# Performance work log

Hardware: AMD Instinct MI355X
Metric: run time of the kernel (lower is better)

Reference implementation:

```python
import jax, jax.numpy as jnp
import numpy as np
import math

D_MODEL = 512
NHEAD = 8
NUM_LAYERS = 3
FF_HIDDEN = 512
B, LQ, LK = 4, 1024, 2048
LN_EPS = 1e-5


def _mha(q_in, k_in, v_in, Wq, Wk, Wv, Wo, nhead, mask):
    # Weights stored [d_in, d_out]; torch Linear(bias=False) is x @ W.T, we fold the
    # transpose into storage so math is identical.
    Bq, Lq, d = q_in.shape
    dh = d // nhead
    # NOTE: original uses .view(B, nhead, -1, dh) on contiguous [B, L, d] — a plain
    # row-major reshape, NOT the usual transpose head split. Replicate exactly.
    q = (q_in @ Wq).reshape(Bq, nhead, -1, dh)
    k = (k_in @ Wk).reshape(Bq, nhead, -1, dh)
    v = (v_in @ Wv).reshape(Bq, nhead, -1, dh)
    u = jnp.einsum('bhqd,bhkd->bhqk', q, k) / math.sqrt(dh)
    if mask is not None:
        m = mask[:, None]  # broadcast over heads
        u = jnp.where(m, -jnp.inf, u)
    attn = jax.nn.softmax(u, axis=-1)
    if mask is not None:
        attn = jnp.where(m, 0.0, attn)
    out = jnp.einsum('bhqk,bhkd->bhqd', attn, v).reshape(Bq, Lq, d)
    return out @ Wo


def _layernorm(x, g, b):
    mu = jnp.mean(x, axis=-1, keepdims=True)
    var = jnp.mean((x - mu) ** 2, axis=-1, keepdims=True)
    return (x - mu) * jax.lax.rsqrt(var + LN_EPS) * g + b


def setup_inputs() -> dict:
    key = jax.random.key(0)
    ks = jax.random.split(key, 16)
    d, L, f = D_MODEL, NUM_LAYERS, FF_HIDDEN
    s = 0.02
    inp = {
        'x': jax.random.normal(ks[0], (B, LK, d), jnp.float32),
        'h': jax.random.normal(ks[1], (B, LQ, d), jnp.float32),
        'mask': jax.random.randint(ks[2], (B, LQ, LK), 0, 10) == 0,
        'wq': jax.random.normal(ks[3], (L, d, d), jnp.float32) * s,
        'wk': jax.random.normal(ks[4], (L, d, d), jnp.float32) * s,
        'wv': jax.random.normal(ks[5], (L, d, d), jnp.float32) * s,
        'wo': jax.random.normal(ks[6], (L, d, d), jnp.float32) * s,
        'ffw1': jax.random.normal(ks[7], (L, d, f), jnp.float32) * s,
        'ffb1': jnp.zeros((L, f), jnp.float32),
        'ffw2': jax.random.normal(ks[8], (L, f, d), jnp.float32) * s,
        'ffb2': jnp.zeros((L, d), jnp.float32),
        'g1': jnp.ones((L, d), jnp.float32),
        'be1': jnp.zeros((L, d), jnp.float32),
        'g2': jnp.ones((L, d), jnp.float32),
        'be2': jnp.zeros((L, d), jnp.float32),
        'out_wq': jax.random.normal(ks[9], (d, d), jnp.float32) * s,
        'out_wk': jax.random.normal(ks[10], (d, d), jnp.float32) * s,
    }
    return inp


def reference(x, h, mask, wq, wk, wv, wo, ffw1, ffb1, ffw2, ffb2, g1, be1, g2, be2, out_wq, out_wk):
    L = wq.shape[0]
    for i in range(L):
        a = _mha(h, x, x, wq[i], wk[i], wv[i], wo[i], NHEAD, mask)
        h = _layernorm(h + a, g1[i], be1[i])
        ff = jax.nn.relu(h @ ffw1[i] + ffb1[i]) @ ffw2[i] + ffb2[i]
        h = _layernorm(h + ff, g2[i], be2[i])
    # output MHA with nhead=1, output_attention=True: returns u.mean(dim=1)
    d = h.shape[-1]
    q = (h @ out_wq)[:, None]  # [B,1,Lq,d]
    k = (x @ out_wk)[:, None]  # [B,1,Lk,d]
    u = jnp.einsum('bhqd,bhkd->bhqk', q, k) / math.sqrt(d)
    # mean over head dim of size 1; torch .squeeze(1) is a no-op since Lq > 1
    return u.mean(axis=1)  # [B, Lq, Lk]
```

## Files before the change

### kernel.cpp

```cpp
#include <hip/hip_runtime.h>
#include <math.h>


#define D_MODEL 512
#define LQ 1024
#define LKK 2048
#define BB 4
#define NL 3
#define KSPLIT 2
#define NROWS 32768
#define WSZC 262144L

typedef __bf16 bf16;
typedef __bf16 bf16x8 __attribute__((ext_vector_type(8)));
typedef __bf16 bf16x4 __attribute__((ext_vector_type(4)));
typedef float f32x4 __attribute__((ext_vector_type(4)));

__device__ inline f32x4 mfma16(bf16x8 a, bf16x8 b, f32x4 c) {
    return __builtin_amdgcn_mfma_f32_16x16x32_bf16(a, b, c, 0, 0, 0);
}

__device__ inline void gload16(const void* g, void* l) {
    __builtin_amdgcn_global_load_lds(
        (const __attribute__((address_space(1))) void*)g,
        (__attribute__((address_space(3))) void*)l, 16, 0, 0);
}

__device__ inline float fexp2(float x) { return __builtin_amdgcn_exp2f(x); }

__global__ __launch_bounds__(256) void cast_kernel(
    const float* __restrict__ in, bf16* __restrict__ out, long n)
{
    long i4 = ((long)blockIdx.x * 256 + threadIdx.x) * 4;
    if (i4 >= n) return;
    float4 v = *(const float4*)(in + i4);
    bf16x4 o;
    o[0] = (bf16)v.x; o[1] = (bf16)v.y; o[2] = (bf16)v.z; o[3] = (bf16)v.w;
    *(bf16x4*)(out + i4) = o;
}

__global__ __launch_bounds__(256) void cast_dual(
    const float* __restrict__ in, float* __restrict__ outf,
    bf16* __restrict__ outb, long n)
{
    long i4 = ((long)blockIdx.x * 256 + threadIdx.x) * 4;
    if (i4 >= n) return;
    float4 v = *(const float4*)(in + i4);
    *(float4*)(outf + i4) = v;
    bf16x4 o;
    o[0] = (bf16)v.x; o[1] = (bf16)v.y; o[2] = (bf16)v.z; o[3] = (bf16)v.w;
    *(bf16x4*)(outb + i4) = o;
}

__global__ __launch_bounds__(256) void tcast_all(
    const float* __restrict__ wq, const float* __restrict__ wo,
    const float* __restrict__ f1, const float* __restrict__ f2,
    const float* __restrict__ wk, const float* __restrict__ wv,
    const float* __restrict__ owq, const float* __restrict__ owk,
    bf16* __restrict__ wts, bf16* __restrict__ wtOQ)
{
    __shared__ float t[32][33];
    int z = blockIdx.z;
    const float* src; bf16* dst;
    if (z < 3)       { src = wq  + z * WSZC;        dst = wts + (long)z * WSZC; }
    else if (z < 6)  { src = wo  + (z - 3) * WSZC;  dst = wts + (long)z * WSZC; }
    else if (z < 9)  { src = f1  + (z - 6) * WSZC;  dst = wts + (long)z * WSZC; }
    else if (z < 12) { src = f2  + (z - 9) * WSZC;  dst = wts + (long)z * WSZC; }
    else if (z < 15) { src = wk  + (z - 12) * WSZC; dst = wts + (12 + 2 * (z - 12)) * WSZC; }
    else if (z < 18) { src = wv  + (z - 15) * WSZC; dst = wts + (13 + 2 * (z - 15)) * WSZC; }
    else if (z == 18){ src = owq;                   dst = wtOQ; }
    else             { src = owk;                   dst = wts + 18 * WSZC; }

    int tx = threadIdx.x & 31, ty = threadIdx.x >> 5;
    int x0 = blockIdx.x * 32, y0 = blockIdx.y * 32;
#pragma unroll
    for (int i = 0; i < 4; i++)
        t[ty + 8 * i][tx] = src[(long)(y0 + ty + 8 * i) * 512 + x0 + tx];
    __syncthreads();
#pragma unroll
    for (int i = 0; i < 4; i++)
        dst[(long)(x0 + ty + 8 * i) * 512 + y0 + tx] = (bf16)t[tx][ty + 8 * i];
}

__global__ __launch_bounds__(256) void maskbits_kernel(
    const int* __restrict__ m, unsigned* __restrict__ bits)
{
    long i = (long)blockIdx.x * 256 + threadIdx.x;
    int v = m[i] != 0;
    unsigned long long bal = __ballot(v);
    int lane = threadIdx.x & 63;
    if (lane == 0) bits[i >> 5] = (unsigned)bal;
    else if (lane == 32) bits[i >> 5] = (unsigned)(bal >> 32);
}

__global__ __launch_bounds__(256) void vtrans_kernel(
    const bf16* __restrict__ v, bf16* __restrict__ vt)
{
    __shared__ bf16 t[64][72];
    int bh = blockIdx.y;
    int p0 = blockIdx.x * 64;
    const bf16* vb = v + ((long)bh * 2048 + p0) * 64;
    bf16* vtb = vt + (long)bh * 64 * 2048;
    int tid = threadIdx.x;
#pragma unroll
    for (int it = 0; it < 2; it++) {
        int r = it * 32 + (tid >> 3);
        int c8 = (tid & 7) * 8;
        bf16x8 vv = *(const bf16x8*)(vb + (long)r * 64 + c8);
        *(bf16x8*)&t[r][c8] = vv;
    }
    __syncthreads();
#pragma unroll
    for (int it = 0; it < 2; it++) {
        int d = it * 32 + (tid >> 3);
        int p8 = (tid & 7) * 8;
        bf16x8 ov;
#pragma unroll
        for (int j = 0; j < 8; j++) ov[j] = t[p8 + j][d];
        *(bf16x8*)(vtb + (long)d * 2048 + p0 + p8) = ov;
    }
}

template<int BIAS, int RELU, int OUT_BF16>
__global__ __launch_bounds__(256) void mfma_gemm(
    const bf16* __restrict__ A, const bf16* __restrict__ Bt,
    const float* __restrict__ bias, void* __restrict__ Cv,
    int N, int K)
{
    __shared__ bf16 As[2][8192];
    __shared__ bf16 Bs[2][4096];
    int tid = threadIdx.x;
    int lane = tid & 63, w = tid >> 6;
    int wr = w >> 1, wc = w & 1;
    int g = lane >> 4, c = lane & 15;
    long row0 = (long)blockIdx.y * 128;
    int n0 = blockIdx.x * 64;

    f32x4 acc[4][2];
#pragma unroll
    for (int m = 0; m < 4; m++)
#pragma unroll
        for (int n = 0; n < 2; n++) acc[m][n] = (f32x4){0.f, 0.f, 0.f, 0.f};

    int lr8 = lane >> 3;
    int scol = ((lane & 7) ^ lr8) * 8;
    int cs = c & 7;

    auto STAGE = [&](int buf, int k0) {
#pragma unroll
        for (int i = 0; i < 4; i++) {
            const bf16* ga = A + (row0 + w * 32 + i * 8 + lr8) * (long)K + k0 + scol;
            gload16(ga, &As[buf][(w * 32 + i * 8) * 64]);
        }
#pragma unroll
        for (int j = 0; j < 2; j++) {
            const bf16* gb = Bt + (long)(n0 + w * 16 + j * 8 + lr8) * K + k0 + scol;
            gload16(gb, &Bs[buf][(w * 16 + j * 8) * 64]);
        }
    };

    STAGE(0, 0);
    __syncthreads();
    int nk = K >> 6;
    for (int it = 0; it < nk; ++it) {
        int cur = it & 1;
        if (it + 1 < nk) STAGE(cur ^ 1, (it + 1) << 6);
#pragma unroll
        for (int kk = 0; kk < 2; kk++) {
            int ch = ((kk << 2) + g);
            bf16x8 af[4], bfr[2];
#pragma unroll
            for (int m = 0; m < 4; m++)
                af[m] = *(const bf16x8*)
                    &As[cur][(wr * 64 + m * 16 + c) * 64 + ((ch ^ cs) << 3)];
#pragma unroll
            for (int n = 0; n < 2; n++)
                bfr[n] = *(const bf16x8*)
                    &Bs[cur][(wc * 32 + n * 16 + c) * 64 + ((ch ^ cs) << 3)];
#pragma unroll
            for (int m = 0; m < 4; m++)
#pragma unroll
                for (int n = 0; n < 2; n++)
                    acc[m][n] = mfma16(af[m], bfr[n], acc[m][n]);
        }
        __syncthreads();
    }

    float bv[2] = {0.f, 0.f};
    if (BIAS) {
#pragma unroll
        for (int n = 0; n < 2; n++) bv[n] = bias[n0 + wc * 32 + n * 16 + c];
    }
    float* Cf = (float*)Cv;
    bf16* Cb = (bf16*)Cv;
#pragma unroll
    for (int m = 0; m < 4; m++)
#pragma unroll
        for (int n = 0; n < 2; n++)
#pragma unroll
            for (int j = 0; j < 4; j++) {
                long row = row0 + wr * 64 + m * 16 + g * 4 + j;
                int col = n0 + wc * 32 + n * 16 + c;
                float v = acc[m][n][j];
                if (BIAS) v += bv[n];
                if (RELU) v = fmaxf(v, 0.f);
                if (OUT_BF16) Cb[row * N + col] = (bf16)v;
                else Cf[row * N + col] = v;
            }
}

template<int OUT_BF16>
__device__ inline void gemm128_body(
    const bf16* __restrict__ Ab, const bf16* __restrict__ Bb,
    void* __restrict__ Cv, int N, int K, float scale,
    long row0, int n0)
{
    __shared__ bf16 As[2][4096];
    __shared__ bf16 Bs[2][4096];
    int tid = threadIdx.x;
    int lane = tid & 63, w = tid >> 6;
    int wr = w >> 1, wc = w & 1;
    int g = lane >> 4, c = lane & 15;

    f32x4 acc[4][4];
#pragma unroll
    for (int m = 0; m < 4; m++)
#pragma unroll
        for (int n = 0; n < 4; n++) acc[m][n] = (f32x4){0.f, 0.f, 0.f, 0.f};

    int lr4 = lane >> 2, lc8 = (lane & 3) * 8;
    auto STAGE = [&](int buf, int k0) {
        const bf16* ga = Ab + (row0 + w * 16 + lr4) * (long)K + k0 + lc8;
        gload16(ga, &As[buf][(w * 16) * 32]);
        gload16(ga + (long)64 * K, &As[buf][(w * 16 + 64) * 32]);
        const bf16* gb = Bb + (long)(n0 + w * 16 + lr4) * K + k0 + lc8;
        gload16(gb, &Bs[buf][(w * 16) * 32]);
        gload16(gb + (long)64 * K, &Bs[buf][(w * 16 + 64) * 32]);
    };

    STAGE(0, 0);
    __syncthreads();
    int nk = K >> 5;
    for (int it = 0; it < nk; ++it) {
        int cur = it & 1;
        if (it + 1 < nk) STAGE(cur ^ 1, (it + 1) << 5);
        bf16x8 af[4], bfr[4];
#pragma unroll
        for (int m = 0; m < 4; m++)
            af[m] = *(const bf16x8*)&As[cur][(wr * 64 + m * 16 + c) * 32 + g * 8];
#pragma unroll
        for (int n = 0; n < 4; n++)
            bfr[n] = *(const bf16x8*)&Bs[cur][(wc * 64 + n * 16 + c) * 32 + g * 8];
#pragma unroll
        for (int m = 0; m < 4; m++)
#pragma unroll
            for (int n = 0; n < 4; n++)
                acc[m][n] = mfma16(af[m], bfr[n], acc[m][n]);
        __syncthreads();
    }

    float* Cf = (float*)Cv;
    bf16* Cb = (bf16*)Cv;
#pragma unroll
    for (int m = 0; m < 4; m++)
#pragma unroll
        for (int n = 0; n < 4; n++)
#pragma unroll
            for (int j = 0; j < 4; j++) {
                long row = row0 + wr * 64 + m * 16 + g * 4 + j;
                int col = n0 + wc * 64 + n * 16 + c;
                float v = acc[m][n][j] * scale;
                if (OUT_BF16) Cb[row * N + col] = (bf16)v;
                else Cf[row * N + col] = v;
            }
}

__global__ __launch_bounds__(256) void mfma_gemm128(
    const bf16* __restrict__ A, const bf16* __restrict__ Bt,
    float* __restrict__ Cv, int N, int K, float scale,
    long sA, long sB, long sC)
{
    long z = blockIdx.z;
    gemm128_body<0>(A + z * sA, Bt + z * sB, Cv + z * sC, N, K, scale,
                    (long)blockIdx.y * 128, blockIdx.x * 128);
}

__global__ __launch_bounds__(256) void qkv_gemm(
    const bf16* __restrict__ Ah, const bf16* __restrict__ Ax,
    const bf16* __restrict__ B0, const bf16* __restrict__ B1,
    const bf16* __restrict__ B2,
    bf16* __restrict__ C0, bf16* __restrict__ C1, bf16* __restrict__ C2,
    float scale0)
{
    int z = blockIdx.z;
    if (z == 0 && blockIdx.y >= 32) return;
    const bf16* A = z ? Ax : Ah;
    const bf16* Bt = (z == 0) ? B0 : (z == 1 ? B1 : B2);
    bf16* C = (z == 0) ? C0 : (z == 1 ? C1 : C2);
    gemm128_body<1>(A, Bt, C, 512, 512, z == 0 ? scale0 : 1.f,
                    (long)blockIdx.y * 128, blockIdx.x * 128);
}

__global__ __launch_bounds__(512, 4) void attn_mfma(
    const bf16* __restrict__ QP, const bf16* __restrict__ KP,
    const bf16* __restrict__ Vt, const unsigned* __restrict__ bits,
    bf16* __restrict__ Opart, float* __restrict__ Mpart,
    float* __restrict__ Lpart)
{
    __shared__ bf16 Kls[2][4096];
    __shared__ bf16 Vls[2][4096];
    __shared__ bf16 Pl[8][1024];

    int tid = threadIdx.x;
    int lane = tid & 63, wv = tid >> 6;
    int g = lane >> 4, c = lane & 15;

    int flat = blockIdx.x;
    int logical = (flat & 7) * 64 + (flat >> 3);
    int bh = logical >> 4;
    int rr = logical & 15;
    int sp = rr >> 3;
    int q0 = (rr & 7) * 128 + wv * 16;
    int b = bh >> 3;

    long qrow0 = (long)bh * 1024 + q0;
    long krow0 = (long)bh * 2048 + (long)sp * 1024;
    const bf16* vtb = Vt + (long)bh * 131072 + (long)sp * 1024;
    const unsigned* bitrow = bits + ((long)b * 1024 + q0 + c) * 64 + sp * 32;

    int lr = lane >> 3, lc = lane & 7;
    int scol = (lc ^ lr) * 8;
    int cs = c & 7;

    bf16x8 qa[2];
#pragma unroll
    for (int hh = 0; hh < 2; hh++)
        qa[hh] = *(const bf16x8*)(QP + (qrow0 + c) * 64 + hh * 32 + g * 8);

    f32x4 o_acc[4];
#pragma unroll
    for (int ot = 0; ot < 4; ot++) o_acc[ot] = (f32x4){0.f, 0.f, 0.f, 0.f};
    float m_r = -1e30f, l_r = 0.f;

    {
        const bf16* sk = KP + (krow0 + wv * 8 + lr) * 64 + scol;
        gload16(sk, &Kls[0][(wv * 8) * 64]);
        const bf16* sv = vtb + (long)(wv * 8 + lr) * 2048 + scol;
        gload16(sv, &Vls[0][(wv * 8) * 64]);
    }
    uint2 wp_nxt = *(const uint2*)(bitrow);
    __syncthreads();

    const int NT = LKK / KSPLIT / 64;
    for (int kt = 0; kt < NT; kt++) {
        int cur = kt & 1;
        if (kt + 1 < NT) {
            int kn = (kt + 1) * 64;
            const bf16* sk = KP + (krow0 + kn + wv * 8 + lr) * 64 + scol;
            gload16(sk, &Kls[cur ^ 1][(wv * 8) * 64]);
            const bf16* sv = vtb + (long)(wv * 8 + lr) * 2048 + kn + scol;
            gload16(sv, &Vls[cur ^ 1][(wv * 8) * 64]);
        }
        uint2 wp = wp_nxt;
        if (kt + 1 < NT) wp_nxt = *(const uint2*)(bitrow + (kt + 1) * 2);

        const char* kls = (const char*)&Kls[cur][0];
        f32x4 s[4];
        __builtin_amdgcn_s_setprio(1);
#pragma unroll
        for (int mt = 0; mt < 4; mt++) {
            bf16x8 ka0 = *(const bf16x8*)(kls + (mt * 16 + c) * 128 + ((g ^ cs) << 4));
            bf16x8 ka1 = *(const bf16x8*)(kls + (mt * 16 + c) * 128 + (((4 + g) ^ cs) << 4));
            s[mt] = mfma16(ka0, qa[0], (f32x4){0.f, 0.f, 0.f, 0.f});
            s[mt] = mfma16(ka1, qa[1], s[mt]);
        }
        __builtin_amdgcn_s_setprio(0);

#pragma unroll
        for (int mt = 0; mt < 4; mt++)
#pragma unroll
            for (int j = 0; j < 4; j++) {
                int kl = mt * 16 + 4 * g + j;
                unsigned wsel = (kl < 32) ? wp.x : wp.y;
                if ((wsel >> (kl & 31)) & 1) s[mt][j] = -1e30f;
            }

        float mxl = -1e30f;
#pragma unroll
        for (int mt = 0; mt < 4; mt++)
            mxl = fmaxf(mxl, fmaxf(fmaxf(s[mt][0], s[mt][1]),
                                   fmaxf(s[mt][2], s[mt][3])));

        float fct = 1.f;
        if (__any(mxl > m_r + 11.5415f)) {
            float mx = fmaxf(mxl, __shfl_xor(mxl, 16, 64));
            mx = fmaxf(mx, __shfl_xor(mx, 32, 64));
            float mnew = fmaxf(m_r, mx);
            fct = fexp2(m_r - mnew);
            m_r = mnew;
            float fq[4];
#pragma unroll
            for (int j = 0; j < 4; j++)
                fq[j] = __shfl(fct, (lane & 48) | (4 * g + j), 64);
#pragma unroll
            for (int ot = 0; ot < 4; ot++)
#pragma unroll
                for (int j = 0; j < 4; j++) o_acc[ot][j] *= fq[j];
        }

        float sum = 0.f;
#pragma unroll
        for (int mt = 0; mt < 4; mt++)
#pragma unroll
            for (int j = 0; j < 4; j++) {
                float p = fexp2(s[mt][j] - m_r);
                s[mt][j] = p;
                sum += p;
            }
        sum += __shfl_xor(sum, 16, 64);
        sum += __shfl_xor(sum, 32, 64);
        l_r = l_r * fct + sum;

        char* plb = (char*)&Pl[wv][0];
#pragma unroll
        for (int mt = 0; mt < 4; mt++) {
            bf16x4 pk;
#pragma unroll
            for (int j = 0; j < 4; j++) pk[j] = (bf16)s[mt][j];
            int wch = (mt * 2 + (g >> 1)) ^ cs;
            *(bf16x4*)(plb + c * 128 + (wch << 4) + (g & 1) * 8) = pk;
        }

        const char* vls = (const char*)&Vls[cur][0];
        __builtin_amdgcn_s_setprio(1);
#pragma unroll
        for (int kh = 0; kh < 2; kh++) {
            bf16x8 pa = *(const bf16x8*)(plb + c * 128 + ((((kh << 2) + g) ^ cs) << 4));
#pragma unroll
            for (int ot = 0; ot < 4; ot++) {
                bf16x8 vbf = *(const bf16x8*)
                    (vls + (ot * 16 + c) * 128 + ((((kh << 2) + g) ^ cs) << 4));
                o_acc[ot] = mfma16(pa, vbf, o_acc[ot]);
            }
        }
        __builtin_amdgcn_s_setprio(0);
        __syncthreads();
    }

    long ob = ((long)sp * NROWS + qrow0) * 64;
#pragma unroll
    for (int ot = 0; ot < 4; ot++)
#pragma unroll
        for (int j = 0; j < 4; j++)
            Opart[ob + (long)(4 * g + j) * 64 + ot * 16 + c] = (bf16)o_acc[ot][j];
    if (g == 0) {
        Mpart[(long)sp * NROWS + qrow0 + c] = m_r;
        Lpart[(long)sp * NROWS + qrow0 + c] = l_r;
    }
}

__global__ __launch_bounds__(256) void attn_combine(
    const bf16* __restrict__ Op, const float* __restrict__ Mp,
    const float* __restrict__ Lp, bf16* __restrict__ O)
{
    long idx = (long)blockIdx.x * 256 + threadIdx.x;
    long row = idx >> 6;
    float m0 = Mp[row], m1 = Mp[NROWS + row];
    float l0 = Lp[row], l1 = Lp[NROWS + row];
    float mm = fmaxf(m0, m1);
    float e0 = fexp2(m0 - mm), e1 = fexp2(m1 - mm);
    float inv = 1.f / (l0 * e0 + l1 * e1);
    float o = ((float)Op[idx] * e0 + (float)Op[(long)NROWS * 64 + idx] * e1) * inv;
    O[idx] = (bf16)o;
}

__global__ __launch_bounds__(256) void ln_kernel(
    const float* __restrict__ res, const float* __restrict__ y,
    const float* __restrict__ g, const float* __restrict__ bb,
    float* __restrict__ outf, bf16* __restrict__ outb)
{
    int wave = threadIdx.x >> 6, lane = threadIdx.x & 63;
    long row = (long)blockIdx.x * 4 + wave;
    const float* rp = res + row * D_MODEL;
    const float* yp = y + row * D_MODEL;
    float v[8];
    float s = 0.f, sq = 0.f;
#pragma unroll
    for (int j = 0; j < 8; j++) {
        int col = lane + 64 * j;
        v[j] = rp[col] + yp[col];
        s += v[j]; sq += v[j] * v[j];
    }
#pragma unroll
    for (int o = 32; o > 0; o >>= 1) {
        s += __shfl_down(s, o, 64);
        sq += __shfl_down(sq, o, 64);
    }
    s = __shfl(s, 0, 64);
    sq = __shfl(sq, 0, 64);
    float mean = s * (1.f / 512.f);
    float var = sq * (1.f / 512.f) - mean * mean;
    float rstd = rsqrtf(fmaxf(var, 0.f) + 1e-5f);
    float* opf = outf + row * D_MODEL;
    bf16* opb = outb + row * D_MODEL;
#pragma unroll
    for (int j = 0; j < 8; j++) {
        int col = lane + 64 * j;
        float o = (v[j] - mean) * rstd * g[col] + bb[col];
        opf[col] = o;
        opb[col] = (bf16)o;
    }
}

extern "C" void kernel_launch(void* const* d_in, const int* in_sizes, int n_in,
                              void* d_out, int out_size, void* d_ws, size_t ws_size,
                              hipStream_t stream)
{
    const float* x    = (const float*)d_in[0];
    const float* hin  = (const float*)d_in[1];
    const int*   mask = (const int*)d_in[2];
    const float* wq   = (const float*)d_in[3];
    const float* wk   = (const float*)d_in[4];
    const float* wv   = (const float*)d_in[5];
    const float* wo   = (const float*)d_in[6];
    const float* ffw1 = (const float*)d_in[7];
    const float* ffb1 = (const float*)d_in[8];
    const float* ffw2 = (const float*)d_in[9];
    const float* ffb2 = (const float*)d_in[10];
    const float* g1   = (const float*)d_in[11];
    const float* be1  = (const float*)d_in[12];
    const float* g2   = (const float*)d_in[13];
    const float* be2  = (const float*)d_in[14];
    const float* out_wq = (const float*)d_in[15];
    const float* out_wk = (const float*)d_in[16];
    float* out = (float*)d_out;

    const long NQ = (long)BB * LQ;
    const long NK = (long)BB * LKK;

    char* W = (char*)d_ws;
    float* h_f  = (float*)(W);
    char*  SH   = W + 8388608;
    float* y_f  = (float*)SH;
    bf16*  v_pl = (bf16*)SH;
    bf16*  opart= (bf16*)SH;
    bf16*  h_b  = (bf16*)(W + 16777216);
    bf16*  x_b  = (bf16*)(W + 20971520);
    bf16*  q_b  = (bf16*)(W + 29360128);
    bf16*  a_b  = (bf16*)(W + 33554432);
    bf16*  k_pl = (bf16*)(W + 37748736);
    bf16*  vt   = (bf16*)(W + 46137344);
    bf16*  wts  = (bf16*)(W + 54525952);
    bf16*  wtOQ = wts + 19 * WSZC;
    unsigned* mb = (unsigned*)(W + 65011712);
    float* Mpart = (float*)(W + 66060288);
    float* Lpart = (float*)(W + 66322432);

    dim3 blk(256);
    dim3 blk512(512);

    cast_kernel<<<dim3((NK * D_MODEL / 4 + 255) / 256), blk, 0, stream>>>(x, x_b, NK * D_MODEL);
    cast_dual<<<dim3((NQ * D_MODEL / 4 + 255) / 256), blk, 0, stream>>>(hin, h_f, h_b, NQ * D_MODEL);
    tcast_all<<<dim3(16, 16, 20), blk, 0, stream>>>(
        wq, wo, ffw1, ffw2, wk, wv, out_wq, out_wk, wts, wtOQ);
    maskbits_kernel<<<dim3(32768), blk, 0, stream>>>(mask, mb);

    dim3 gq(8, 32, 1);
    dim3 gqkv(4, 64, 3);
    dim3 gvt(32, 32);
    dim3 ga(512);
    dim3 gc(NROWS * 64 / 256);

    const float C2 = 0.1803368801111243f;

    for (int i = 0; i < NL; i++) {
        qkv_gemm<<<gqkv, blk, 0, stream>>>(h_b, x_b,
            wts + i * WSZC, wts + (12 + 2 * i) * WSZC, wts + (13 + 2 * i) * WSZC,
            q_b, k_pl, v_pl, C2);
        vtrans_kernel<<<gvt, blk, 0, stream>>>(v_pl, vt);

        attn_mfma<<<ga, blk512, 0, stream>>>(q_b, k_pl, vt, mb, opart, Mpart, Lpart);
        attn_combine<<<gc, blk, 0, stream>>>(opart, Mpart, Lpart, a_b);

        mfma_gemm<0,0,0><<<gq, blk, 0, stream>>>(a_b, wts + (3 + i) * WSZC,
            nullptr, y_f, 512, 512);
        ln_kernel<<<dim3(NQ / 4), blk, 0, stream>>>(h_f, y_f,
            g1 + i * D_MODEL, be1 + i * D_MODEL, h_f, h_b);

        mfma_gemm<1,1,1><<<gq, blk, 0, stream>>>(h_b, wts + (6 + i) * WSZC,
            ffb1 + i * D_MODEL, q_b, 512, 512);
        mfma_gemm<1,0,0><<<gq, blk, 0, stream>>>(q_b, wts + (9 + i) * WSZC,
            ffb2 + i * D_MODEL, y_f, 512, 512);
        ln_kernel<<<dim3(NQ / 4), blk, 0, stream>>>(h_f, y_f,
            g2 + i * D_MODEL, be2 + i * D_MODEL, h_f, h_b);
    }

    dim3 gqk(4, 64, 2);
    qkv_gemm<<<gqk, blk, 0, stream>>>(h_b, x_b,
        wtOQ, wts + 18 * WSZC, wts + 18 * WSZC, q_b, k_pl, k_pl, 1.f);

    dim3 gf(LKK / 128, LQ / 128, BB);
    mfma_gemm128<<<gf, blk, 0, stream>>>(q_b, k_pl, out,
        LKK, 512, 0.04419417382415922f,
        (long)LQ * 512, (long)LKK * 512, (long)LQ * LKK);
}
```

Measured before the change: 397.1 us.

## Deepen GEMM K-tile with swizzled LDS and defer attention row-sum reduction

```diff
diff --git a/kernel.cpp b/kernel.cpp
--- a/kernel.cpp
+++ b/kernel.cpp
@@ -215,8 +215,8 @@
     void* __restrict__ Cv, int N, int K, float scale,
     long row0, int n0)
 {
-    __shared__ bf16 As[2][4096];
-    __shared__ bf16 Bs[2][4096];
+    __shared__ bf16 As[2][8192];
+    __shared__ bf16 Bs[2][8192];
     int tid = threadIdx.x;
     int lane = tid & 63, w = tid >> 6;
     int wr = w >> 1, wc = w & 1;
@@ -228,34 +228,44 @@
 #pragma unroll
         for (int n = 0; n < 4; n++) acc[m][n] = (f32x4){0.f, 0.f, 0.f, 0.f};
 
-    int lr4 = lane >> 2, lc8 = (lane & 3) * 8;
+    int lr8 = lane >> 3;
+    int scol = ((lane & 7) ^ lr8) * 8;
+    int cs = c & 7;
+
     auto STAGE = [&](int buf, int k0) {
-        const bf16* ga = Ab + (row0 + w * 16 + lr4) * (long)K + k0 + lc8;
-        gload16(ga, &As[buf][(w * 16) * 32]);
-        gload16(ga + (long)64 * K, &As[buf][(w * 16 + 64) * 32]);
-        const bf16* gb = Bb + (long)(n0 + w * 16 + lr4) * K + k0 + lc8;
-        gload16(gb, &Bs[buf][(w * 16) * 32]);
-        gload16(gb + (long)64 * K, &Bs[buf][(w * 16 + 64) * 32]);
+#pragma unroll
+        for (int i = 0; i < 4; i++) {
+            const bf16* ga = Ab + (row0 + w * 32 + i * 8 + lr8) * (long)K + k0 + scol;
+            gload16(ga, &As[buf][(w * 32 + i * 8) * 64]);
+            const bf16* gb = Bb + (long)(n0 + w * 32 + i * 8 + lr8) * K + k0 + scol;
+            gload16(gb, &Bs[buf][(w * 32 + i * 8) * 64]);
+        }
     };
 
     STAGE(0, 0);
     __syncthreads();
-    int nk = K >> 5;
+    int nk = K >> 6;
     for (int it = 0; it < nk; ++it) {
         int cur = it & 1;
-        if (it + 1 < nk) STAGE(cur ^ 1, (it + 1) << 5);
-        bf16x8 af[4], bfr[4];
-#pragma unroll
-        for (int m = 0; m < 4; m++)
-            af[m] = *(const bf16x8*)&As[cur][(wr * 64 + m * 16 + c) * 32 + g * 8];
-#pragma unroll
-        for (int n = 0; n < 4; n++)
-            bfr[n] = *(const bf16x8*)&Bs[cur][(wc * 64 + n * 16 + c) * 32 + g * 8];
-#pragma unroll
-        for (int m = 0; m < 4; m++)
+        if (it + 1 < nk) STAGE(cur ^ 1, (it + 1) << 6);
+#pragma unroll
+        for (int kk = 0; kk < 2; kk++) {
+            int ch = ((kk << 2) + g);
+            bf16x8 af[4], bfr[4];
+#pragma unroll
+            for (int m = 0; m < 4; m++)
+                af[m] = *(const bf16x8*)
+                    &As[cur][(wr * 64 + m * 16 + c) * 64 + ((ch ^ cs) << 3)];
 #pragma unroll
             for (int n = 0; n < 4; n++)
-                acc[m][n] = mfma16(af[m], bfr[n], acc[m][n]);
+                bfr[n] = *(const bf16x8*)
+                    &Bs[cur][(wc * 64 + n * 16 + c) * 64 + ((ch ^ cs) << 3)];
+#pragma unroll
+            for (int m = 0; m < 4; m++)
+#pragma unroll
+                for (int n = 0; n < 4; n++)
+                    acc[m][n] = mfma16(af[m], bfr[n], acc[m][n]);
+        }
         __syncthreads();
     }
 
@@ -377,13 +387,12 @@
         __builtin_amdgcn_s_setprio(0);
 
 #pragma unroll
-        for (int mt = 0; mt < 4; mt++)
-#pragma unroll
-            for (int j = 0; j < 4; j++) {
-                int kl = mt * 16 + 4 * g + j;
-                unsigned wsel = (kl < 32) ? wp.x : wp.y;
-                if ((wsel >> (kl & 31)) & 1) s[mt][j] = -1e30f;
-            }
+        for (int mt = 0; mt < 4; mt++) {
+            unsigned wm = ((mt < 2) ? wp.x : wp.y) >> ((mt & 1) * 16 + 4 * g);
+#pragma unroll
+            for (int j = 0; j < 4; j++)
+                if ((wm >> j) & 1) s[mt][j] = -1e30f;
+        }
 
         float mxl = -1e30f;
 #pragma unroll
@@ -417,8 +426,6 @@
                 s[mt][j] = p;
                 sum += p;
             }
-        sum += __shfl_xor(sum, 16, 64);
-        sum += __shfl_xor(sum, 32, 64);
         l_r = l_r * fct + sum;
 
         char* plb = (char*)&Pl[wv][0];
@@ -446,6 +453,9 @@
         __builtin_amdgcn_s_setprio(0);
         __syncthreads();
     }
+
+    l_r += __shfl_xor(l_r, 16, 64);
+    l_r += __shfl_xor(l_r, 32, 64);
 
     long ob = ((long)sp * NROWS + qrow0) * 64;
 #pragma unroll
```

After: 401.0 us. About the same (+1.0%).
